# Optimization experiments

Measured on AMD Instinct MI355X. Metric: run time of the kernel, lower is better.

The kernel has to match this reference:

```python
import jax, jax.numpy as jnp
import numpy as np

GROUPS = 32
EPS = 1e-5
NUM_HEADS = 8
HEAD_DIM = 64
CHANNELS = 512


def group_norm(x, scale, bias):
    # x: [b, h, w, c]; normalize over (h, w, channels-within-group)
    b, h, w, c = x.shape
    xg = x.reshape(b, h, w, GROUPS, c // GROUPS)
    mean = jnp.mean(xg, axis=(1, 2, 4), keepdims=True)
    var = jnp.var(xg, axis=(1, 2, 4), keepdims=True)
    xg = (xg - mean) * jax.lax.rsqrt(var + EPS)
    return xg.reshape(b, h, w, c) * scale + bias


def setup_inputs() -> dict:
    key = jax.random.key(0)
    ks = jax.random.split(key, 8)
    b, hs, ws, c = 8, 32, 32, CHANNELS
    inner = NUM_HEADS * HEAD_DIM
    return {
        "x": jax.random.normal(ks[0], (b, hs, ws, c), dtype=jnp.float32),
        "t": jax.random.normal(ks[1], (b,), dtype=jnp.float32),
        "gn_scale": jnp.ones((c,), dtype=jnp.float32),
        "gn_bias": jnp.zeros((c,), dtype=jnp.float32),
        "w_qkv": jax.random.normal(ks[2], (c, 3 * inner), dtype=jnp.float32) * 0.02,
        "b_qkv": jnp.zeros((3 * inner,), dtype=jnp.float32),
        "w_out": jax.random.normal(ks[3], (inner, c), dtype=jnp.float32) * 0.02,
        "b_out": jnp.zeros((c,), dtype=jnp.float32),
    }


def reference(x, t, gn_scale, gn_bias, w_qkv, b_qkv, w_out, b_out):
    b, hs, ws, c = x.shape
    # NOTE: original reassigns x = GroupNorm(x); the residual uses the NORMALIZED x.
    xn = group_norm(x, gn_scale, gn_bias)
    x_flat = xn.reshape(b, hs * ws, c)                      # [b, s, c]
    qkv = x_flat @ w_qkv + b_qkv                            # [b, s, 3*nh*hd]
    qkv = qkv.reshape(b, hs * ws, NUM_HEADS, 3 * HEAD_DIM)
    q, k, v = jnp.split(qkv, 3, axis=-1)                    # each [b, s, nh, hd]
    q = q / jnp.sqrt(jnp.float32(HEAD_DIM))
    q = q.transpose(0, 2, 1, 3)                             # [b, nh, s, hd]
    k = k.transpose(0, 2, 1, 3)
    v = v.transpose(0, 2, 1, 3)
    attn = jax.nn.softmax(jnp.einsum('bhqd,bhkd->bhqk', q, k), axis=-1)
    out = jnp.einsum('bhqk,bhkd->bhqd', attn, v)            # [b, nh, s, hd]
    out = out.transpose(0, 2, 1, 3).reshape(b, hs * ws, NUM_HEADS * HEAD_DIM)
    h = out @ w_out + b_out                                 # [b, s, c]
    h = h.reshape(b, hs, ws, c)
    return xn + h
```

## Files before the change

kernel.cpp:

```cpp
#include <hip/hip_runtime.h>
#include <hip/hip_bf16.h>


#define B_    8
#define S_    1024
#define C_    512
#define NH    8
#define HD    64
#define QKVC  1536
#define GROUPS 32
#define GSIZE  16
#define EPSV   1e-5f
#define QSCL  0.18033688f

using frag8 = __attribute__((ext_vector_type(8))) short;
using f32x4 = __attribute__((ext_vector_type(4))) float;

__device__ __forceinline__ float bf2f(unsigned short u) {
    union { unsigned int i; float f; } v; v.i = ((unsigned int)u) << 16; return v.f;
}
__device__ __forceinline__ unsigned short f2bf(float f) {
    union { float f; unsigned int i; } v; v.f = f;
    unsigned int x = v.i;
    return (unsigned short)((x + 0x7fffu + ((x >> 16) & 1u)) >> 16);
}
__device__ __forceinline__ unsigned int pk2bf(float a, float b) {
    union { float f; unsigned int u; } x, y; x.f = a; y.f = b;
    return __builtin_amdgcn_perm(y.u + 0x8000u, x.u + 0x8000u, 0x07060302u);
}
__device__ __forceinline__ float fexp2(float x) {
#if __has_builtin(__builtin_amdgcn_exp2f)
    return __builtin_amdgcn_exp2f(x);
#else
    return exp2f(x);
#endif
}
__device__ __forceinline__ f32x4 zero4() {
    f32x4 z; z[0] = 0.f; z[1] = 0.f; z[2] = 0.f; z[3] = 0.f; return z;
}
__device__ __forceinline__ void gl_lds(const unsigned short* gp, unsigned short* lp) {
    __builtin_amdgcn_global_load_lds(
        (const __attribute__((address_space(1))) void*)gp,
        (__attribute__((address_space(3))) void*)lp, 16, 0, 0);
}

__global__ __launch_bounds__(256) void prep_kernel(
        const float* __restrict__ w_qkv, const float* __restrict__ w_out,
        unsigned short* __restrict__ wqkvT, unsigned short* __restrict__ woutT,
        const float* __restrict__ x,
        const float* __restrict__ scale, const float* __restrict__ bias,
        unsigned short* __restrict__ xn) {
    __shared__ unsigned short xcache[16384];
    __shared__ float s_red[8];
    int id = blockIdx.x;
    int t = threadIdx.x;
    if (id < 1024) {
        float* tile = (float*)xcache;
        const float* in; unsigned short* out; int N, n0, k0;
        if (id < 768) { in = w_qkv; out = wqkvT; N = QKVC; n0 = (id % 48) * 32; k0 = (id / 48) * 32; }
        else { int i2 = id - 768; in = w_out; out = woutT; N = C_; n0 = (i2 % 16) * 32; k0 = (i2 / 16) * 32; }
        for (int i = 0; i < 4; ++i) {
            int idx = t + i * 256; int r = idx >> 5, c = idx & 31;
            tile[r * 33 + c] = in[(size_t)(k0 + r) * N + n0 + c];
        }
        __syncthreads();
        for (int i = 0; i < 2; ++i) {
            int idx = t + i * 256;
            int r = idx >> 4, c2 = (idx & 15) * 2;
            unsigned int pk = pk2bf(tile[c2 * 33 + r], tile[(c2 + 1) * 33 + r]);
            *(unsigned int*)(&out[(size_t)(n0 + r) * C_ + k0 + c2]) = pk;
        }
        return;
    }
    int s = id - 1024;
    int xcd = s & 7, u = s >> 3;
    int gp = xcd * 16 + (u >> 1);
    int b = gp >> 4, g = ((gp & 15) << 1) | (u & 1);
    const float* xb = x + (size_t)b * S_ * C_;

    float sum = 0.f, ss = 0.f;
    for (int i = 0; i < 16; ++i) {
        int idx = t + i * 256;
        int row = idx >> 2, j = idx & 3;
        float4 v = *(const float4*)(xb + (size_t)row * C_ + g * GSIZE + j * 4);
        sum += v.x + v.y + v.z + v.w;
        ss  += v.x * v.x + v.y * v.y + v.z * v.z + v.w * v.w;
        uint2 c;
        c.x = pk2bf(v.x, v.y);
        c.y = pk2bf(v.z, v.w);
        *(uint2*)(&xcache[idx * 4]) = c;
    }
    for (int off = 1; off < 64; off <<= 1) {
        sum += __shfl_xor(sum, off);
        ss  += __shfl_xor(ss,  off);
    }
    int wid = t >> 6;
    if ((t & 63) == 0) { s_red[wid] = sum; s_red[4 + wid] = ss; }
    __syncthreads();
    sum = s_red[0] + s_red[1] + s_red[2] + s_red[3];
    ss  = s_red[4] + s_red[5] + s_red[6] + s_red[7];
    float mean = sum * (1.f / 16384.f);
    float var  = ss * (1.f / 16384.f) - mean * mean;
    float rinv = rsqrtf(var + EPSV);

    float sc[16], bi[16];
    for (int u2 = 0; u2 < 16; ++u2) {
        sc[u2] = scale[g * GSIZE + u2];
        bi[u2] = bias[g * GSIZE + u2];
    }
    for (int i = 0; i < 16; ++i) {
        int idx = t + i * 256;
        int row = idx >> 2, j = idx & 3;
        uint2 c = *(const uint2*)(&xcache[idx * 4]);
        float v0 = bf2f((unsigned short)(c.x & 0xffffu));
        float v1 = bf2f((unsigned short)(c.x >> 16));
        float v2 = bf2f((unsigned short)(c.y & 0xffffu));
        float v3 = bf2f((unsigned short)(c.y >> 16));
        int c0 = j * 4;
        float f0 = (v0 - mean) * rinv * sc[c0 + 0] + bi[c0 + 0];
        float f1 = (v1 - mean) * rinv * sc[c0 + 1] + bi[c0 + 1];
        float f2 = (v2 - mean) * rinv * sc[c0 + 2] + bi[c0 + 2];
        float f3 = (v3 - mean) * rinv * sc[c0 + 3] + bi[c0 + 3];
        uint2 o;
        o.x = pk2bf(f0, f1);
        o.y = pk2bf(f2, f3);
        *(uint2*)(xn + (size_t)b * S_ * C_ + (size_t)row * C_ + g * GSIZE + c0) = o;
    }
}

__global__ __launch_bounds__(256) void gemm_qkv_kernel(
        const unsigned short* __restrict__ A,
        const unsigned short* __restrict__ Bt,
        const float* __restrict__ bias,
        unsigned short* __restrict__ outA,
        unsigned short* __restrict__ outV) {
    __shared__ unsigned short As[2][128 * 32];
    __shared__ unsigned short Bs[2][128 * 32];
    unsigned int flat = blockIdx.y * 12u + blockIdx.x;
    unsigned int nid = (flat & 7u) * 96u + (flat >> 3);
    int my = nid / 12u, mx = nid % 12u;
    int m0 = my * 128, n0 = mx * 128;
    int t = threadIdx.x;
    int wid = t >> 6, lane = t & 63;
    int quad = lane >> 4, l16 = lane & 15;
    int wm = (wid >> 1) * 64, wn = (wid & 1) * 64;

    f32x4 acc[4][4];
    for (int mi = 0; mi < 4; ++mi)
        for (int ni = 0; ni < 4; ++ni) acc[mi][ni] = zero4();

    int srow = t >> 2;
    int sseg_sw = (t & 3) ^ ((t >> 3) & 3);
    auto stage = [&](int k0, int buf) {
        for (int i = 0; i < 2; ++i) {
            gl_lds(A + (size_t)(m0 + i * 64 + srow) * C_ + k0 + sseg_sw * 8,
                   &As[buf][(size_t)(i * 256 + wid * 64) * 8]);
            gl_lds(Bt + (size_t)(n0 + i * 64 + srow) * C_ + k0 + sseg_sw * 8,
                   &Bs[buf][(size_t)(i * 256 + wid * 64) * 8]);
        }
    };

    int rsw8 = ((l16 >> 1) & 3) * 8;

    stage(0, 0);
    const int nk = C_ >> 5;
    for (int i = 0; i < nk; ++i) {
        __syncthreads();
        if (i + 1 < nk) stage((i + 1) << 5, (i + 1) & 1);
        int buf = i & 1;

        frag8 bfrag[4], afrag[4];
        for (int ni = 0; ni < 4; ++ni)
            bfrag[ni] = *(const frag8*)(&Bs[buf][(wn + ni * 16 + l16) * 32 + ((quad * 8) ^ rsw8)]);
        for (int mi = 0; mi < 4; ++mi)
            afrag[mi] = *(const frag8*)(&As[buf][(wm + mi * 16 + l16) * 32 + ((quad * 8) ^ rsw8)]);

        for (int mi = 0; mi < 4; ++mi)
            for (int ni = 0; ni < 4; ++ni)
                acc[mi][ni] = __builtin_amdgcn_mfma_f32_16x16x32_bf16(
                    afrag[mi], bfrag[ni], acc[mi][ni], 0, 0, 0);
    }

    for (int ni = 0; ni < 4; ++ni) {
        int c0 = n0 + wn + ni * 16;
        float bv = bias[c0 + l16];
        int h = c0 / 192, rr = c0 % 192;
        if (rr >= 128) {
            int d = rr - 128 + l16;
            int bidx = m0 >> 10;
            unsigned short* vp = outV + (((size_t)bidx * NH + h) * HD + d) * S_
                               + (m0 & 1023) + wm + quad * 4;
            for (int mi = 0; mi < 4; ++mi) {
                uint2 pk;
                pk.x = pk2bf(acc[mi][ni][0] + bv, acc[mi][ni][1] + bv);
                pk.y = pk2bf(acc[mi][ni][2] + bv, acc[mi][ni][3] + bv);
                *(uint2*)(vp + mi * 16) = pk;
            }
        } else {
            float scl = (rr < 64) ? QSCL : 1.0f;
            int colk = h * 128 + rr + l16;
            for (int mi = 0; mi < 4; ++mi)
                for (int r = 0; r < 4; ++r) {
                    int row = m0 + wm + mi * 16 + quad * 4 + r;
                    outA[(size_t)row * 1024 + colk] = f2bf((acc[mi][ni][r] + bv) * scl);
                }
        }
    }
}

__global__ __launch_bounds__(256) void gemm_out_kernel(
        const unsigned short* __restrict__ A,
        const unsigned short* __restrict__ Bt,
        const float* __restrict__ bias,
        const unsigned short* __restrict__ resid,
        float* __restrict__ outF) {
    __shared__ unsigned short As[2][2][64 * 32];
    __shared__ unsigned short Bs[2][2][128 * 32];
    unsigned int flat = blockIdx.x;
    unsigned int nid = (flat & 7u) * 64u + (flat >> 3);
    int my = nid >> 2, mx = nid & 3;
    int m0 = my * 64, n0 = mx * 128;
    int t = threadIdx.x;
    int wid = t >> 6, lane = t & 63;
    int quad = lane >> 4, l16 = lane & 15;
    int wm = (wid >> 1) * 32, wn = (wid & 1) * 64;

    f32x4 acc[2][4];
    for (int mi = 0; mi < 2; ++mi)
        for (int ni = 0; ni < 4; ++ni) acc[mi][ni] = zero4();

    int srow = t >> 2;
    int sseg_sw = (t & 3) ^ ((t >> 3) & 3);
    auto stage = [&](int k0, int buf) {
        for (int s = 0; s < 2; ++s) {
            gl_lds(A + (size_t)(m0 + srow) * C_ + k0 + s * 32 + sseg_sw * 8,
                   &As[buf][s][(size_t)wid * 512]);
            for (int i = 0; i < 2; ++i)
                gl_lds(Bt + (size_t)(n0 + i * 64 + srow) * C_ + k0 + s * 32 + sseg_sw * 8,
                       &Bs[buf][s][(size_t)(i * 256 + wid * 64) * 8]);
        }
    };

    int rsw8 = ((l16 >> 1) & 3) * 8;

    stage(0, 0);
    const int nk = C_ >> 6;
    for (int i = 0; i < nk; ++i) {
        __syncthreads();
        if (i + 1 < nk) stage((i + 1) << 6, (i + 1) & 1);
        int buf = i & 1;

        for (int s = 0; s < 2; ++s) {
            frag8 bfrag[4], afrag[2];
            for (int ni = 0; ni < 4; ++ni)
                bfrag[ni] = *(const frag8*)(&Bs[buf][s][(wn + ni * 16 + l16) * 32 + ((quad * 8) ^ rsw8)]);
            for (int mi = 0; mi < 2; ++mi)
                afrag[mi] = *(const frag8*)(&As[buf][s][(wm + mi * 16 + l16) * 32 + ((quad * 8) ^ rsw8)]);

            for (int mi = 0; mi < 2; ++mi)
                for (int ni = 0; ni < 4; ++ni)
                    acc[mi][ni] = __builtin_amdgcn_mfma_f32_16x16x32_bf16(
                        afrag[mi], bfrag[ni], acc[mi][ni], 0, 0, 0);
        }
    }

    for (int ni = 0; ni < 4; ++ni) {
        int col = n0 + wn + ni * 16 + l16;
        float bv = bias[col];
        for (int mi = 0; mi < 2; ++mi)
            for (int r = 0; r < 4; ++r) {
                int row = m0 + wm + mi * 16 + quad * 4 + r;
                float v = acc[mi][ni][r] + bv + bf2f(resid[(size_t)row * C_ + col]);
                outF[(size_t)row * C_ + col] = v;
            }
    }
}

__global__ __launch_bounds__(256) void attn_kernel(
        const unsigned short* __restrict__ kq,
        const unsigned short* __restrict__ vT,
        unsigned short* __restrict__ attn_out) {
    int i = blockIdx.x;
    int xcd = i & 7, slot = i >> 3;
    int bh = xcd * 8 + (slot >> 3);
    int qt = slot & 7;
    int b = bh >> 3, h = bh & 7;

    int t = threadIdx.x;
    int wid = t >> 6, lane = t & 63, quad = lane >> 4, l16 = lane & 15;
    int q0 = qt * 128 + wid * 32;

    __shared__ unsigned short Ks[2][2][2048];
    __shared__ unsigned short Vs[2][2][2048];

    const unsigned short* qrow0 = kq + ((size_t)b * S_ + q0 + l16) * 1024 + h * 128;
    const unsigned short* qrow1 = qrow0 + (size_t)16 * 1024;
    frag8 qf[2][2];
    qf[0][0] = *(const frag8*)(qrow0 + quad * 8);
    qf[0][1] = *(const frag8*)(qrow0 + 32 + quad * 8);
    qf[1][0] = *(const frag8*)(qrow1 + quad * 8);
    qf[1][1] = *(const frag8*)(qrow1 + 32 + quad * 8);

    f32x4 o[2][4];
    float lsum[2] = {0.f, 0.f};
    for (int g = 0; g < 2; ++g)
        for (int dt = 0; dt < 4; ++dt) o[g][dt] = zero4();

    const unsigned short* kbase = kq + (size_t)b * S_ * 1024 + h * 128 + 64;
    const unsigned short* vbase = vT + ((size_t)b * NH + h) * HD * S_;

    int kdh = wid & 1, krh = wid >> 1;
    int krow = krh * 16 + (lane >> 2);
    int kseg = (lane & 3) ^ ((lane >> 3) & 3);
    int vd = wid * 16 + (lane >> 2);
    int vseg = lane & 3;
    int vkh = vseg >> 1, vsp = vseg & 1;
    int vsw = (lane >> 3) & 3;
    int vo1 = (((vsp * 2) ^ vsw) * 8) + vkh * 4;
    int vo2 = (((vsp * 2 + 1) ^ vsw) * 8) + vkh * 4;

    int ksw = (l16 >> 1) & 3;

    auto stageK = [&](int j0, int buf, int half) {
        gl_lds(kbase + (size_t)(j0 + krow) * 1024 + kdh * 32 + kseg * 8,
               &Ks[buf][half][kdh * 1024 + krh * 512]);
    };
    auto loadV = [&](int j0) {
        return *(const uint4*)(vbase + (size_t)vd * S_ + j0 + vseg * 8);
    };
    auto writeV = [&](uint4 w, int buf, int half) {
        unsigned short* vdst = &Vs[buf][half][vd * 32];
        uint2 g1; g1.x = w.x; g1.y = w.y;
        uint2 g2; g2.x = w.z; g2.y = w.w;
        *(uint2*)(vdst + vo1) = g1;
        *(uint2*)(vdst + vo2) = g2;
    };

    stageK(0, 0, 0);  stageK(32, 0, 1);
    writeV(loadV(0), 0, 0);  writeV(loadV(32), 0, 1);

    for (int it = 0; it < S_ / 64; ++it) {
        int cur = it & 1, nxt = cur ^ 1;
        __syncthreads();
        uint4 vn0, vn1;
        bool more = (it < S_ / 64 - 1);
        if (more) {
            int jn = (it + 1) * 64;
            stageK(jn, nxt, 0);
            stageK(jn + 32, nxt, 1);
            vn0 = loadV(jn);
            vn1 = loadV(jn + 32);
        }

        for (int half = 0; half < 2; ++half) {
            frag8 kf[2][2];
            for (int kh = 0; kh < 2; ++kh)
                for (int dh = 0; dh < 2; ++dh)
                    kf[kh][dh] = *(const frag8*)(&Ks[cur][half][dh * 1024
                        + (kh * 16 + l16) * 32 + ((quad ^ ksw) * 8)]);

            frag8 vf[4];
            for (int dt = 0; dt < 4; ++dt)
                vf[dt] = *(const frag8*)(&Vs[cur][half][(dt * 16 + l16) * 32
                        + ((quad ^ ksw) * 8)]);

            for (int g = 0; g < 2; ++g) {
                f32x4 s0 = zero4(), s1 = zero4();
                __builtin_amdgcn_s_setprio(1);
                s0 = __builtin_amdgcn_mfma_f32_16x16x32_bf16(kf[0][0], qf[g][0], s0, 0, 0, 0);
                s0 = __builtin_amdgcn_mfma_f32_16x16x32_bf16(kf[0][1], qf[g][1], s0, 0, 0, 0);
                s1 = __builtin_amdgcn_mfma_f32_16x16x32_bf16(kf[1][0], qf[g][0], s1, 0, 0, 0);
                s1 = __builtin_amdgcn_mfma_f32_16x16x32_bf16(kf[1][1], qf[g][1], s1, 0, 0, 0);
                __builtin_amdgcn_s_setprio(0);

                union { frag8 f; unsigned int u[4]; } pfu;
                pfu.u[0] = pk2bf(fexp2(s0[0]), fexp2(s0[1]));
                pfu.u[1] = pk2bf(fexp2(s0[2]), fexp2(s0[3]));
                pfu.u[2] = pk2bf(fexp2(s1[0]), fexp2(s1[1]));
                pfu.u[3] = pk2bf(fexp2(s1[2]), fexp2(s1[3]));

                float lacc = 0.f;
#pragma unroll
                for (int w2 = 0; w2 < 4; ++w2) {
                    union { unsigned int u; float f; } plo, phi;
                    plo.u = pfu.u[w2] << 16;
                    phi.u = pfu.u[w2] & 0xffff0000u;
                    lacc += plo.f + phi.f;
                }
                lsum[g] += lacc;

                __builtin_amdgcn_s_setprio(1);
                for (int dt = 0; dt < 4; ++dt)
                    o[g][dt] = __builtin_amdgcn_mfma_f32_16x16x32_bf16(pfu.f, vf[dt], o[g][dt], 0, 0, 0);
                __builtin_amdgcn_s_setprio(0);
            }
        }

        if (more) {
            writeV(vn0, nxt, 0);
            writeV(vn1, nxt, 1);
        }
    }

    for (int g = 0; g < 2; ++g) {
        float lq = lsum[g];
        lq += __shfl_xor(lq, 16);
        lq += __shfl_xor(lq, 32);
        for (int r = 0; r < 4; ++r) {
            float inv = 1.0f / __shfl(lq, quad * 4 + r);
            int qrw = q0 + g * 16 + quad * 4 + r;
            for (int dt = 0; dt < 4; ++dt) {
                int ch = h * HD + dt * 16 + l16;
                attn_out[((size_t)b * S_ + qrw) * C_ + ch] = f2bf(o[g][dt][r] * inv);
            }
        }
    }
}

extern "C" void kernel_launch(void* const* d_in, const int* in_sizes, int n_in,
                              void* d_out, int out_size, void* d_ws, size_t ws_size,
                              hipStream_t stream) {
    const float* x        = (const float*)d_in[0];
    const float* gn_scale = (const float*)d_in[2];
    const float* gn_bias  = (const float*)d_in[3];
    const float* w_qkv    = (const float*)d_in[4];
    const float* b_qkv    = (const float*)d_in[5];
    const float* w_out    = (const float*)d_in[6];
    const float* b_out    = (const float*)d_in[7];
    float* out = (float*)d_out;

    char* ws = (char*)d_ws;
    unsigned short* xn    = (unsigned short*)(ws);
    unsigned short* kq    = (unsigned short*)(ws + ((size_t)8  << 20));
    unsigned short* attn  = (unsigned short*)(ws + ((size_t)24 << 20));
    unsigned short* vT    = (unsigned short*)(ws + ((size_t)32 << 20));
    unsigned short* wqkvT = (unsigned short*)(ws + ((size_t)40 << 20));
    unsigned short* woutT = (unsigned short*)(ws + ((size_t)40 << 20) + ((size_t)3 << 19));

    prep_kernel<<<dim3(1280), 256, 0, stream>>>(
        w_qkv, w_out, wqkvT, woutT, x, gn_scale, gn_bias, xn);

    gemm_qkv_kernel<<<dim3(QKVC / 128, (B_ * S_) / 128), 256, 0, stream>>>(
        xn, wqkvT, b_qkv, kq, vT);

    attn_kernel<<<dim3(512), 256, 0, stream>>>(kq, vT, attn);

    gemm_out_kernel<<<dim3(512), 256, 0, stream>>>(
        attn, woutT, b_out, xn, out);
}
```

Baseline: 147.9 us.

## Load GEMM B-operand fragments directly from global into registers, bypassing LDS

Both the QKV and output-projection GEMMs stop staging the weight (B) tile through shared memory. Each wave now loads its B fragments straight from global memory into register double buffers. The main loop is unrolled by two so register buffers alternate. This frees LDS, adds an occupancy hint of 3 blocks on the QKV kernel, and removes the LDS round-trip for B. The cost is duplicated global loads across waves that share columns and more register pressure.

Result: slower. 167.3 us (+13.1%).

```diff
diff --git a/kernel.cpp b/kernel.cpp
--- a/kernel.cpp
+++ b/kernel.cpp
@@ -128,14 +128,13 @@
     }
 }
 
-__global__ __launch_bounds__(256) void gemm_qkv_kernel(
+__global__ __launch_bounds__(256, 3) void gemm_qkv_kernel(
         const unsigned short* __restrict__ A,
         const unsigned short* __restrict__ Bt,
         const float* __restrict__ bias,
         unsigned short* __restrict__ outA,
         unsigned short* __restrict__ outV) {
     __shared__ unsigned short As[2][128 * 32];
-    __shared__ unsigned short Bs[2][128 * 32];
     unsigned int flat = blockIdx.y * 12u + blockIdx.x;
     unsigned int nid = (flat & 7u) * 96u + (flat >> 3);
     int my = nid / 12u, mx = nid % 12u;
@@ -151,34 +150,45 @@
 
     int srow = t >> 2;
     int sseg_sw = (t & 3) ^ ((t >> 3) & 3);
-    auto stage = [&](int k0, int buf) {
-        for (int i = 0; i < 2; ++i) {
+    auto stageA = [&](int k0, int buf) {
+        for (int i = 0; i < 2; ++i)
             gl_lds(A + (size_t)(m0 + i * 64 + srow) * C_ + k0 + sseg_sw * 8,
                    &As[buf][(size_t)(i * 256 + wid * 64) * 8]);
-            gl_lds(Bt + (size_t)(n0 + i * 64 + srow) * C_ + k0 + sseg_sw * 8,
-                   &Bs[buf][(size_t)(i * 256 + wid * 64) * 8]);
-        }
+    };
+
+    const unsigned short* bbase = Bt + (size_t)(n0 + wn + l16) * C_ + quad * 8;
+    frag8 bA[4], bB[4];
+    auto loadB = [&](int k0, frag8* d) {
+#pragma unroll
+        for (int ni = 0; ni < 4; ++ni)
+            d[ni] = *(const frag8*)(bbase + (size_t)(ni * 16) * C_ + k0);
     };
 
     int rsw8 = ((l16 >> 1) & 3) * 8;
 
-    stage(0, 0);
-    const int nk = C_ >> 5;
-    for (int i = 0; i < nk; ++i) {
-        __syncthreads();
-        if (i + 1 < nk) stage((i + 1) << 5, (i + 1) & 1);
-        int buf = i & 1;
-
-        frag8 bfrag[4], afrag[4];
-        for (int ni = 0; ni < 4; ++ni)
-            bfrag[ni] = *(const frag8*)(&Bs[buf][(wn + ni * 16 + l16) * 32 + ((quad * 8) ^ rsw8)]);
+    auto compute = [&](int buf, frag8* bf) {
+        frag8 afrag[4];
+#pragma unroll
         for (int mi = 0; mi < 4; ++mi)
             afrag[mi] = *(const frag8*)(&As[buf][(wm + mi * 16 + l16) * 32 + ((quad * 8) ^ rsw8)]);
-
+#pragma unroll
         for (int mi = 0; mi < 4; ++mi)
+#pragma unroll
             for (int ni = 0; ni < 4; ++ni)
                 acc[mi][ni] = __builtin_amdgcn_mfma_f32_16x16x32_bf16(
-                    afrag[mi], bfrag[ni], acc[mi][ni], 0, 0, 0);
+                    afrag[mi], bf[ni], acc[mi][ni], 0, 0, 0);
+    };
+
+    stageA(0, 0);
+    loadB(0, bA);
+    const int nk = C_ >> 5;
+    for (int i = 0; i < nk; i += 2) {
+        __syncthreads();
+        if (i + 1 < nk) { stageA((i + 1) << 5, 1); loadB((i + 1) << 5, bB); }
+        compute(0, bA);
+        __syncthreads();
+        if (i + 2 < nk) { stageA((i + 2) << 5, 0); loadB((i + 2) << 5, bA); }
+        compute(1, bB);
     }
 
     for (int ni = 0; ni < 4; ++ni) {
@@ -215,7 +225,6 @@
         const unsigned short* __restrict__ resid,
         float* __restrict__ outF) {
     __shared__ unsigned short As[2][2][64 * 32];
-    __shared__ unsigned short Bs[2][2][128 * 32];
     unsigned int flat = blockIdx.x;
     unsigned int nid = (flat & 7u) * 64u + (flat >> 3);
     int my = nid >> 2, mx = nid & 3;
@@ -231,37 +240,51 @@
 
     int srow = t >> 2;
     int sseg_sw = (t & 3) ^ ((t >> 3) & 3);
-    auto stage = [&](int k0, int buf) {
-        for (int s = 0; s < 2; ++s) {
+    auto stageA = [&](int k0, int buf) {
+#pragma unroll
+        for (int s = 0; s < 2; ++s)
             gl_lds(A + (size_t)(m0 + srow) * C_ + k0 + s * 32 + sseg_sw * 8,
                    &As[buf][s][(size_t)wid * 512]);
-            for (int i = 0; i < 2; ++i)
-                gl_lds(Bt + (size_t)(n0 + i * 64 + srow) * C_ + k0 + s * 32 + sseg_sw * 8,
-                       &Bs[buf][s][(size_t)(i * 256 + wid * 64) * 8]);
-        }
+    };
+
+    const unsigned short* bbase = Bt + (size_t)(n0 + wn + l16) * C_ + quad * 8;
+    frag8 bA[2][4], bB[2][4];
+    auto loadB = [&](int k0, frag8 (*d)[4]) {
+#pragma unroll
+        for (int s = 0; s < 2; ++s)
+#pragma unroll
+            for (int ni = 0; ni < 4; ++ni)
+                d[s][ni] = *(const frag8*)(bbase + (size_t)(ni * 16) * C_ + k0 + s * 32);
     };
 
     int rsw8 = ((l16 >> 1) & 3) * 8;
 
-    stage(0, 0);
-    const int nk = C_ >> 6;
-    for (int i = 0; i < nk; ++i) {
-        __syncthreads();
-        if (i + 1 < nk) stage((i + 1) << 6, (i + 1) & 1);
-        int buf = i & 1;
-
+    auto compute = [&](int buf, frag8 (*bf)[4]) {
+#pragma unroll
         for (int s = 0; s < 2; ++s) {
-            frag8 bfrag[4], afrag[2];
-            for (int ni = 0; ni < 4; ++ni)
-                bfrag[ni] = *(const frag8*)(&Bs[buf][s][(wn + ni * 16 + l16) * 32 + ((quad * 8) ^ rsw8)]);
+            frag8 afrag[2];
+#pragma unroll
             for (int mi = 0; mi < 2; ++mi)
                 afrag[mi] = *(const frag8*)(&As[buf][s][(wm + mi * 16 + l16) * 32 + ((quad * 8) ^ rsw8)]);
-
+#pragma unroll
             for (int mi = 0; mi < 2; ++mi)
+#pragma unroll
                 for (int ni = 0; ni < 4; ++ni)
                     acc[mi][ni] = __builtin_amdgcn_mfma_f32_16x16x32_bf16(
-                        afrag[mi], bfrag[ni], acc[mi][ni], 0, 0, 0);
-        }
+                        afrag[mi], bf[s][ni], acc[mi][ni], 0, 0, 0);
+        }
+    };
+
+    stageA(0, 0);
+    loadB(0, bA);
+    const int nk = C_ >> 6;
+    for (int i = 0; i < nk; i += 2) {
+        __syncthreads();
+        if (i + 1 < nk) { stageA((i + 1) << 6, 1); loadB((i + 1) << 6, bB); }
+        compute(0, bA);
+        __syncthreads();
+        if (i + 2 < nk) { stageA((i + 2) << 6, 0); loadB((i + 2) << 6, bA); }
+        compute(1, bB);
     }
 
     for (int ni = 0; ni < 4; ++ni) {
```
